# Optimization experiments

Hardware: AMD Instinct MI355X
Metric: run time of the kernel (lower is better)

## Reference

```python
import jax, jax.numpy as jnp
import numpy as np

ALPHA = 0.2  # LeakyReLU negative slope
NEG_BIG = -9e15


def setup_inputs() -> dict:
    key = jax.random.key(0)
    k1, k2, k3, k4 = jax.random.split(key, 4)
    B, N, F_in, F_out = 8, 2048, 256, 256
    x = jax.random.normal(k1, (B, N, F_in), dtype=jnp.float32)
    adj = jax.random.randint(k2, (B, N, N), 0, 2, dtype=jnp.int32)
    # Xavier-uniform init like nn.init.xavier_uniform_
    limW = float(np.sqrt(6.0 / (F_in + F_out)))
    W = jax.random.uniform(k3, (F_in, F_out), minval=-limW, maxval=limW, dtype=jnp.float32)
    lima = float(np.sqrt(6.0 / (2 * F_out + 1)))
    a = jax.random.uniform(k4, (2 * F_out, 1), minval=-lima, maxval=lima, dtype=jnp.float32)
    return {"x": x, "adj": adj, "W": W, "a": a}


def reference(x, adj, W, a):
    # x: (B,N,Fin), adj: (B,N,N), W: (Fin,Fout), a: (2*Fout,1)
    F_out = W.shape[1]
    Wh = jnp.einsum('bnf,fo->bno', x, W)            # (B,N,Fout)
    a1, a2 = a[:F_out, 0], a[F_out:, 0]
    # e[b,i,j] = leakyrelu(Wh[b,i]@a1 + Wh[b,j]@a2)  (equivalent to concat+matmul)
    e = (Wh @ a1)[:, :, None] + (Wh @ a2)[:, None, :]  # (B,N,N)
    e = jnp.where(e > 0, e, ALPHA * e)
    attention = jnp.where(adj > 0, e, NEG_BIG)
    attention = jax.nn.softmax(attention, axis=-1)
    # dropout is identity in eval mode (training=False)
    h_prime = jnp.einsum('bij,bjo->bio', attention, Wh)  # (B,N,Fout)
    return jax.nn.elu(h_prime)  # concat=True -> ELU
```

## Files before the change

kernel.cpp:

```cpp
#include <hip/hip_runtime.h>
#include <hip/hip_fp16.h>

typedef _Float16 f16;
typedef _Float16 half4 __attribute__((ext_vector_type(4)));
typedef _Float16 half8 __attribute__((ext_vector_type(8)));
typedef float f32x4 __attribute__((ext_vector_type(4)));

#define BATCH 8
#define NTOK 2048
#define FIN 256
#define FOUT 256
#define ALPHA 0.2f


__device__ __forceinline__ void gload16(const void* g, void* l) {
    __builtin_amdgcn_global_load_lds(
        (const __attribute__((address_space(1))) unsigned int*)(g),
        (__attribute__((address_space(3))) unsigned int*)(l), 16, 0, 0);
}

__global__ void k_wt(const float* __restrict__ W, f16* __restrict__ WT) {
    __shared__ float t[32][33];
    int o0 = blockIdx.x * 32, k0 = blockIdx.y * 32;
    int tx = threadIdx.x, ty = threadIdx.y;
    t[ty][tx] = W[(k0 + ty) * FOUT + o0 + tx];
    __syncthreads();
    WT[(o0 + ty) * FIN + (k0 + tx)] = (f16)t[tx][ty];
}

__global__ __launch_bounds__(256) void k_pack(const int* __restrict__ adj,
                                              unsigned long long* __restrict__ mask) {
    int t = threadIdx.x;
    int lane = t & 63, w = t >> 6;
    int wid = blockIdx.x * 4 + w;
    const int* base0 = adj + (size_t)wid * 8192;
    unsigned long long* mdst = mask + (size_t)wid * 128;
    for (int it = 0; it < 8; it++) {
        const int* base = base0 + it * 1024;
        int v[16];
#pragma unroll
        for (int k = 0; k < 16; k++) v[k] = base[k * 64 + lane];
        unsigned long long mv[16];
#pragma unroll
        for (int k = 0; k < 16; k++) mv[k] = __ballot(v[k] > 0);
        if (lane < 16) {
            unsigned long long r = mv[0];
#pragma unroll
            for (int k = 1; k < 16; k++) r = (lane == k) ? mv[k] : r;
            mdst[it * 16 + lane] = r;
        }
    }
}

__global__ __launch_bounds__(256) void k_gemm(const float* __restrict__ x,
                                              const f16* __restrict__ WT,
                                              const float* __restrict__ a,
                                              f16* __restrict__ WhT,
                                              float* __restrict__ s1,
                                              float* __restrict__ s2) {
    __shared__ __align__(16) char gsmem[46080];
    int t = threadIdx.x;
    int lane = t & 63, w = t >> 6;
    f16* Ah = (f16*)gsmem;
    f16* Bt = (f16*)(gsmem + 9216);
    int m0 = blockIdx.x * 64;
    int lr = lane & 15, lg = lane >> 4;
    f32x4 acc[4][4] = {};

    for (int k0 = 0; k0 < FIN; k0 += 64) {
        {
            int r = t >> 2, c = (t & 3) * 16;
            const float* src = x + (size_t)(m0 + r) * FIN + k0 + c;
            f32x4 v0 = *(const f32x4*)(src);
            f32x4 v1 = *(const f32x4*)(src + 4);
            f32x4 v2 = *(const f32x4*)(src + 8);
            f32x4 v3 = *(const f32x4*)(src + 12);
            half8 h0, h1;
#pragma unroll
            for (int q = 0; q < 4; q++) {
                h0[q] = (f16)v0[q]; h0[q + 4] = (f16)v1[q];
                h1[q] = (f16)v2[q]; h1[q + 4] = (f16)v3[q];
            }
            f16* dst = Ah + r * 72 + c;
            *(half8*)dst = h0;
            *(half8*)(dst + 8) = h1;
        }
        {
            const f16* src = WT + (size_t)t * FIN + k0;
            f16* dst = Bt + t * 72;
#pragma unroll
            for (int q = 0; q < 8; q++)
                *(half8*)(dst + q * 8) = *(const half8*)(src + q * 8);
        }
        __syncthreads();
#pragma unroll
        for (int kc = 0; kc < 2; kc++) {
            int krow = kc * 32 + lg * 8;
            half8 af[4], bf[4];
#pragma unroll
            for (int fi = 0; fi < 4; fi++)
                af[fi] = *(half8*)(Ah + (fi * 16 + lr) * 72 + krow);
#pragma unroll
            for (int fo = 0; fo < 4; fo++)
                bf[fo] = *(half8*)(Bt + (w * 64 + fo * 16 + lr) * 72 + krow);
#pragma unroll
            for (int fi = 0; fi < 4; fi++)
#pragma unroll
                for (int fo = 0; fo < 4; fo++)
                    acc[fi][fo] = __builtin_amdgcn_mfma_f32_16x16x32_f16(
                        af[fi], bf[fo], acc[fi][fo], 0, 0, 0);
        }
        __syncthreads();
    }

    int b = m0 >> 11;
    int slab_i = (m0 & (NTOK - 1)) >> 6;
    int nbase = m0 & (NTOK - 1);

    float* sred = (float*)gsmem;
    f16* slab = (f16*)(gsmem + 9216);
    float a1v[4], a2v[4];
#pragma unroll
    for (int fo = 0; fo < 4; fo++) {
        int o = w * 64 + fo * 16 + lr;
        a1v[fo] = a[o];
        a2v[fo] = a[FOUT + o];
    }
#pragma unroll
    for (int fi = 0; fi < 4; fi++) {
        f32x4 p1 = {}, p2 = {};
#pragma unroll
        for (int fo = 0; fo < 4; fo++) {
            p1 += acc[fi][fo] * a1v[fo];
            p2 += acc[fi][fo] * a2v[fo];
        }
#pragma unroll
        for (int q = 0; q < 4; q++) {
#pragma unroll
            for (int d = 1; d < 16; d <<= 1) {
                p1[q] += __shfl_xor(p1[q], d);
                p2[q] += __shfl_xor(p2[q], d);
            }
        }
        if (lr == 0) {
            int row = fi * 16 + lg * 4;
#pragma unroll
            for (int q = 0; q < 4; q++) {
                sred[w * 64 + row + q] = p1[q];
                sred[256 + w * 64 + row + q] = p2[q];
            }
        }
    }
#pragma unroll
    for (int fi = 0; fi < 4; fi++) {
        int jg8 = fi * 2 + (lg >> 1), jq0 = (lg & 1) * 4;
#pragma unroll
        for (int fo = 0; fo < 4; fo++) {
            int o = w * 64 + fo * 16 + lr;
            half4 hv;
#pragma unroll
            for (int q = 0; q < 4; q++) hv[q] = (f16)acc[fi][fo][q];
            *(half4*)(slab + o * 64 + ((jg8 ^ (o & 7)) * 8) + jq0) = hv;
        }
    }
    __syncthreads();

    if (t < 64) {
        s1[(size_t)b * NTOK + nbase + t] =
            sred[t] + sred[64 + t] + sred[128 + t] + sred[192 + t];
    } else if (t < 128) {
        int r2 = t - 64;
        s2[(size_t)b * NTOK + nbase + r2] =
            sred[256 + r2] + sred[320 + r2] + sred[384 + r2] + sred[448 + r2];
    }
    {
        const int4* sl = (const int4*)slab;
        int4* gd = (int4*)(WhT + ((size_t)(b * 32 + slab_i) * 256) * 64);
#pragma unroll
        for (int i = 0; i < 8; i++) gd[i * 256 + t] = sl[i * 256 + t];
    }
}

__global__ __launch_bounds__(512, 2) void k_attn(const unsigned* __restrict__ mask32,
                                                 const f16* __restrict__ WhT,
                                                 const float* __restrict__ s1g,
                                                 const float* __restrict__ s2g,
                                                 float* __restrict__ out) {
    __shared__ __align__(16) char smem[65536 + 8192 + 512 + 64];
    f16* Bl = (f16*)smem;
    float* s2_lds = (float*)(smem + 65536);
    float* lpart = (float*)(smem + 65536 + 8192);
    float* wmax = (float*)(smem + 65536 + 8192 + 512);

    int b = blockIdx.x & 7;
    int i0 = (blockIdx.x >> 3) * 64;
    int t = threadIdx.x;
    int lane = t & 63, w = t >> 6;
    int js = w & 1, oh = (w >> 1) & 1, rg = w >> 2;
    int lr = lane & 15, lg = lane >> 4;

    {
        f32x4 sv4 = ((const f32x4*)(s2g + (size_t)b * NTOK))[t];
        ((f32x4*)s2_lds)[t] = sv4;
        float tmx = fmaxf(fmaxf(sv4[0], sv4[1]), fmaxf(sv4[2], sv4[3]));
#pragma unroll
        for (int d = 1; d < 64; d <<= 1) tmx = fmaxf(tmx, __shfl_xor(tmx, d));
        if (lane == 0) wmax[w] = tmx;
    }

    const char* wsrc = (const char*)WhT + (size_t)b * (32 * 32768);
    {
        const char* src = wsrc + (w * 4) * 1024 + lane * 16;
        char* dst = (char*)Bl + (w * 4) * 1024;
#pragma unroll
        for (int k = 0; k < 4; k++) gload16(src + k * 1024, dst + k * 1024);
    }

    int r0 = i0 + rg * 32 + lr, r1 = r0 + 16;
    float s1r0 = s1g[(size_t)b * NTOK + r0];
    float s1r1 = s1g[(size_t)b * NTOK + r1];
    const unsigned* mr0 = mask32 + (size_t)(b * NTOK + r0) * 64 + js;
    const unsigned* mr1 = mask32 + (size_t)(b * NTOK + r1) * 64 + js;

    f32x4 acc0[8] = {}, acc1[8] = {};
    float l0 = 0.f, l1 = 0.f;
    int rswz = ((js * 4 + lg) ^ (lr & 7)) * 8;

    unsigned bw0 = mr0[0], bw1 = mr1[0];

    __syncthreads();

    float s2m = wmax[0];
#pragma unroll
    for (int k = 1; k < 8; k++) s2m = fmaxf(s2m, wmax[k]);
    float tx0 = s1r0 + s2m;
    float mx0 = fmaxf(tx0, ALPHA * tx0);
    float tx1 = s1r1 + s2m;
    float mx1 = fmaxf(tx1, ALPHA * tx1);

    for (int s = 0; s < 32; s++) {
        int buf = s & 1;
        if (s < 31) {
            const char* src = wsrc + (size_t)(s + 1) * 32768 + (w * 4) * 1024 + lane * 16;
            char* dst = (char*)Bl + (buf ^ 1) * 32768 + (w * 4) * 1024;
#pragma unroll
            for (int k = 0; k < 4; k++) gload16(src + k * 1024, dst + k * 1024);
        }

        unsigned cw0 = bw0, cw1 = bw1;
        if (s < 31) { bw0 = mr0[(s + 1) * 2]; bw1 = mr1[(s + 1) * 2]; }
        unsigned bits0 = (cw0 >> (lg * 8)) & 0xffu;
        unsigned bits1 = (cw1 >> (lg * 8)) & 0xffu;

        int sb = s * 64 + js * 32 + lg * 8;
        f32x4 sA = *(const f32x4*)&s2_lds[sb];
        f32x4 sB = *(const f32x4*)&s2_lds[sb + 4];

        half8 ph0, ph1;
#pragma unroll
        for (int q = 0; q < 8; q++) {
            float sv = q < 4 ? sA[q & 3] : sB[q & 3];
            float sx = s1r0 + sv;
            float ev = fmaxf(sx, ALPHA * sx);
            float p = ((bits0 >> q) & 1) ? __expf(ev - mx0) : 0.f;
            l0 += p; ph0[q] = (f16)p;
            float sy = s1r1 + sv;
            float eu = fmaxf(sy, ALPHA * sy);
            float u = ((bits1 >> q) & 1) ? __expf(eu - mx1) : 0.f;
            l1 += u; ph1[q] = (f16)u;
        }

        const f16* bbase = Bl + buf * 16384 + (oh * 128 + lr) * 64 + rswz;
#pragma unroll
        for (int ot = 0; ot < 8; ot++) {
            half8 bf = *(const half8*)(bbase + ot * (16 * 64));
            acc0[ot] = __builtin_amdgcn_mfma_f32_16x16x32_f16(ph0, bf, acc0[ot], 0, 0, 0);
            acc1[ot] = __builtin_amdgcn_mfma_f32_16x16x32_f16(ph1, bf, acc1[ot], 0, 0, 0);
        }
        __syncthreads();
    }

    l0 += __shfl_xor(l0, 16); l0 += __shfl_xor(l0, 32);
    l1 += __shfl_xor(l1, 16); l1 += __shfl_xor(l1, 32);
    if (oh == 0 && lg == 0) {
        lpart[js * 64 + rg * 32 + lr] = l0;
        lpart[js * 64 + rg * 32 + 16 + lr] = l1;
    }
    __syncthreads();

    float* accx = (float*)smem;
    if (js == 1) {
#pragma unroll
        for (int ot = 0; ot < 8; ot++)
#pragma unroll
            for (int q = 0; q < 4; q++) {
                accx[(rg * 32 + lg * 4 + q) * 260 + oh * 128 + ot * 16 + lr] = acc0[ot][q];
                accx[(rg * 32 + 16 + lg * 4 + q) * 260 + oh * 128 + ot * 16 + lr] = acc1[ot][q];
            }
    }
    __syncthreads();
    if (js == 0) {
        f32x4 rl0, rl1;
#pragma unroll
        for (int q = 0; q < 4; q++) {
            int ra = rg * 32 + lg * 4 + q, rb = ra + 16;
            rl0[q] = 1.f / (lpart[ra] + lpart[64 + ra]);
            rl1[q] = 1.f / (lpart[rb] + lpart[64 + rb]);
        }
#pragma unroll
        for (int ot = 0; ot < 8; ot++) {
            int o = oh * 128 + ot * 16 + lr;
#pragma unroll
            for (int q = 0; q < 4; q++) {
                int ra = rg * 32 + lg * 4 + q;
                float u = (acc0[ot][q] + accx[ra * 260 + o]) * rl0[q];
                u = u > 0.f ? u : __expf(u) - 1.f;
                __builtin_nontemporal_store(u, &out[((size_t)(b * NTOK + i0 + ra)) * FOUT + o]);
                int rb = ra + 16;
                float v = (acc1[ot][q] + accx[rb * 260 + o]) * rl1[q];
                v = v > 0.f ? v : __expf(v) - 1.f;
                __builtin_nontemporal_store(v, &out[((size_t)(b * NTOK + i0 + rb)) * FOUT + o]);
            }
        }
    }
}

extern "C" void kernel_launch(void* const* d_in, const int* in_sizes, int n_in,
                              void* d_out, int out_size, void* d_ws, size_t ws_size,
                              hipStream_t stream) {
    const float* x = (const float*)d_in[0];
    const int* adj = (const int*)d_in[1];
    const float* W = (const float*)d_in[2];
    const float* a = (const float*)d_in[3];
    float* out = (float*)d_out;

    char* ws = (char*)d_ws;
    f16* WT = (f16*)ws;
    f16* WhT = (f16*)(ws + 131072);
    float* s1 = (float*)(ws + 131072 + 8388608);
    float* s2 = s1 + BATCH * NTOK;
    unsigned long long* mask64 =
        (unsigned long long*)(ws + 131072 + 8388608 + 196608);

    k_wt<<<dim3(FOUT / 32, FIN / 32), dim3(32, 32), 0, stream>>>(W, WT);
    k_gemm<<<dim3(BATCH * NTOK / 64), 256, 0, stream>>>(x, WT, a, WhT, s1, s2);
    k_pack<<<dim3(1024), 256, 0, stream>>>(adj, mask64);
    k_attn<<<dim3(BATCH * NTOK / 64), 512, 0, stream>>>((const unsigned*)mask64, WhT,
                                                        s1, s2, out);
}
```

Measured before the change: 91.19 us.

## Fuse adjacency bit-packing into attention kernel via LDS mask tile

Removes the separate k_pack kernel and its global mask buffer. Each attention block now reads its own 64 rows of the int32 adjacency matrix directly, packs them into 32-bit masks in LDS, and reads the masks from LDS inside the main loop. This drops one kernel launch and the mask round trip through global memory. In exchange the LDS footprint grows to about 91KB, so launch bounds drop to one block per CU, which lowers occupancy, and the 128MB adjacency read now sits serially before the attention loop in each block.

```diff
diff --git a/kernel.cpp b/kernel.cpp
--- a/kernel.cpp
+++ b/kernel.cpp
@@ -26,30 +26,6 @@
     t[ty][tx] = W[(k0 + ty) * FOUT + o0 + tx];
     __syncthreads();
     WT[(o0 + ty) * FIN + (k0 + tx)] = (f16)t[tx][ty];
-}
-
-__global__ __launch_bounds__(256) void k_pack(const int* __restrict__ adj,
-                                              unsigned long long* __restrict__ mask) {
-    int t = threadIdx.x;
-    int lane = t & 63, w = t >> 6;
-    int wid = blockIdx.x * 4 + w;
-    const int* base0 = adj + (size_t)wid * 8192;
-    unsigned long long* mdst = mask + (size_t)wid * 128;
-    for (int it = 0; it < 8; it++) {
-        const int* base = base0 + it * 1024;
-        int v[16];
-#pragma unroll
-        for (int k = 0; k < 16; k++) v[k] = base[k * 64 + lane];
-        unsigned long long mv[16];
-#pragma unroll
-        for (int k = 0; k < 16; k++) mv[k] = __ballot(v[k] > 0);
-        if (lane < 16) {
-            unsigned long long r = mv[0];
-#pragma unroll
-            for (int k = 1; k < 16; k++) r = (lane == k) ? mv[k] : r;
-            mdst[it * 16 + lane] = r;
-        }
-    }
 }
 
 __global__ __launch_bounds__(256) void k_gemm(const float* __restrict__ x,
@@ -181,16 +157,17 @@
     }
 }
 
-__global__ __launch_bounds__(512, 2) void k_attn(const unsigned* __restrict__ mask32,
+__global__ __launch_bounds__(512, 1) void k_attn(const int* __restrict__ adj,
                                                  const f16* __restrict__ WhT,
                                                  const float* __restrict__ s1g,
                                                  const float* __restrict__ s2g,
                                                  float* __restrict__ out) {
-    __shared__ __align__(16) char smem[65536 + 8192 + 512 + 64];
+    __shared__ __align__(16) char smem[91264];
     f16* Bl = (f16*)smem;
     float* s2_lds = (float*)(smem + 65536);
-    float* lpart = (float*)(smem + 65536 + 8192);
-    float* wmax = (float*)(smem + 65536 + 8192 + 512);
+    unsigned* mask_lds = (unsigned*)(smem + 73728);
+    float* lpart = (float*)(smem + 90624);
+    float* wmax = (float*)(smem + 91136);
 
     int b = blockIdx.x & 7;
     int i0 = (blockIdx.x >> 3) * 64;
@@ -216,17 +193,39 @@
         for (int k = 0; k < 4; k++) gload16(src + k * 1024, dst + k * 1024);
     }
 
-    int r0 = i0 + rg * 32 + lr, r1 = r0 + 16;
+    {
+        const int4* abase = (const int4*)(adj + ((size_t)(b * NTOK + i0 + w * 8)) * NTOK)
+                            + lane * 8;
+        int4 cur[8], nxt[8];
+#pragma unroll
+        for (int k = 0; k < 8; k++) cur[k] = abase[k];
+        for (int r = 0; r < 8; r++) {
+            if (r < 7) {
+#pragma unroll
+                for (int k = 0; k < 8; k++) nxt[k] = abase[(r + 1) * 512 + k];
+            }
+            unsigned m = 0;
+#pragma unroll
+            for (int k = 0; k < 8; k++) {
+                m |= (unsigned)(cur[k].x > 0) << (k * 4);
+                m |= (unsigned)(cur[k].y > 0) << (k * 4 + 1);
+                m |= (unsigned)(cur[k].z > 0) << (k * 4 + 2);
+                m |= (unsigned)(cur[k].w > 0) << (k * 4 + 3);
+            }
+            mask_lds[(w * 8 + r) * 66 + lane] = m;
+#pragma unroll
+            for (int k = 0; k < 8; k++) cur[k] = nxt[k];
+        }
+    }
+
+    int rr0 = rg * 32 + lr;
+    int r0 = i0 + rr0, r1 = r0 + 16;
     float s1r0 = s1g[(size_t)b * NTOK + r0];
     float s1r1 = s1g[(size_t)b * NTOK + r1];
-    const unsigned* mr0 = mask32 + (size_t)(b * NTOK + r0) * 64 + js;
-    const unsigned* mr1 = mask32 + (size_t)(b * NTOK + r1) * 64 + js;
 
     f32x4 acc0[8] = {}, acc1[8] = {};
     float l0 = 0.f, l1 = 0.f;
     int rswz = ((js * 4 + lg) ^ (lr & 7)) * 8;
-
-    unsigned bw0 = mr0[0], bw1 = mr1[0];
 
     __syncthreads();
 
@@ -247,8 +246,8 @@
             for (int k = 0; k < 4; k++) gload16(src + k * 1024, dst + k * 1024);
         }
 
-        unsigned cw0 = bw0, cw1 = bw1;
-        if (s < 31) { bw0 = mr0[(s + 1) * 2]; bw1 = mr1[(s + 1) * 2]; }
+        unsigned cw0 = mask_lds[rr0 * 66 + s * 2 + js];
+        unsigned cw1 = mask_lds[(rr0 + 16) * 66 + s * 2 + js];
         unsigned bits0 = (cw0 >> (lg * 8)) & 0xffu;
         unsigned bits1 = (cw1 >> (lg * 8)) & 0xffu;
 
@@ -339,12 +338,8 @@
     f16* WhT = (f16*)(ws + 131072);
     float* s1 = (float*)(ws + 131072 + 8388608);
     float* s2 = s1 + BATCH * NTOK;
-    unsigned long long* mask64 =
-        (unsigned long long*)(ws + 131072 + 8388608 + 196608);
 
     k_wt<<<dim3(FOUT / 32, FIN / 32), dim3(32, 32), 0, stream>>>(W, WT);
     k_gemm<<<dim3(BATCH * NTOK / 64), 256, 0, stream>>>(x, WT, a, WhT, s1, s2);
-    k_pack<<<dim3(1024), 256, 0, stream>>>(adj, mask64);
-    k_attn<<<dim3(BATCH * NTOK / 64), 512, 0, stream>>>((const unsigned*)mask64, WhT,
-                                                        s1, s2, out);
-}
+    k_attn<<<dim3(BATCH * NTOK / 64), 512, 0, stream>>>(adj, WhT, s1, s2, out);
+}
```

Measured after the change: 82.85 us. 9.1% less time.
